# Kernel tuning notes

Measured on AMD Instinct MI355X. Metric: run time of the kernel, lower is better.

## Reference

```python
import jax, jax.numpy as jnp
import numpy as np

# Sizes: N news nodes, E 'similar' edges, 768-d input, hidden 64, 4 heads, 2 HGT layers, 2 classes
N, E, F_IN, HID, H, L, C = 100000, 1600000, 768, 64, 4, 2, 2
D = HID // H  # per-head dim = 16


def setup_inputs() -> dict:
    key = jax.random.key(0)
    ks = jax.random.split(key, 16)
    s = 0.05
    nrm = lambda k, shape: jax.random.normal(k, shape, jnp.float32) * s
    return {
        "x": jax.random.normal(ks[0], (N, F_IN), jnp.float32),
        "edge_index": jax.random.randint(ks[1], (2, E), 0, N, jnp.int32),
        # input projection
        "Wp": nrm(ks[2], (F_IN, HID)), "bp": jnp.zeros((HID,), jnp.float32),
        # per-layer HGT params (stacked over L layers)
        "Wk": nrm(ks[3], (L, HID, HID)), "bk": jnp.zeros((L, HID), jnp.float32),
        "Wq": nrm(ks[4], (L, HID, HID)), "bq": jnp.zeros((L, HID), jnp.float32),
        "Wv": nrm(ks[5], (L, HID, HID)), "bv": jnp.zeros((L, HID), jnp.float32),
        "a_rel": nrm(ks[6], (L, H, D, D)),  # per-edge-type attention transform
        "m_rel": nrm(ks[7], (L, H, D, D)),  # per-edge-type message transform
        "p_rel": jnp.ones((L, H), jnp.float32),  # relation prior
        "Wo": nrm(ks[8], (L, HID, HID)), "bo": jnp.zeros((L, HID), jnp.float32),
        "skip": jnp.ones((L,), jnp.float32),
        # classifier MLP: 64 -> 32 -> 2
        "Wc1": nrm(ks[9], (HID, HID // 2)), "bc1": jnp.zeros((HID // 2,), jnp.float32),
        "Wc2": nrm(ks[10], (HID // 2, C)), "bc2": jnp.zeros((C,), jnp.float32),
    }


def _hgt_layer(h, src, dst, Wk, bk, Wq, bq, Wv, bv, a_rel, m_rel, p_rel, Wo, bo, skip):
    n = h.shape[0]
    k = (h @ Wk + bk).reshape(n, H, D)
    q = (h @ Wq + bq).reshape(n, H, D)
    v = (h @ Wv + bv).reshape(n, H, D)
    # per-edge attention logits: (k_src @ a_rel) . q_dst * p_rel / sqrt(D)
    k_e = jnp.einsum('ehd,hdf->ehf', k[src], a_rel)          # [E,H,D]
    alpha = jnp.einsum('ehf,ehf->eh', k_e, q[dst]) * p_rel / np.float32(np.sqrt(D))
    # segment softmax over incoming edges of each dst node
    mx = jax.ops.segment_max(alpha, dst, num_segments=n)     # [N,H]
    a = jnp.exp(alpha - mx[dst])
    denom = jax.ops.segment_sum(a, dst, num_segments=n)
    a = a / (denom[dst] + 1e-16)
    # messages + scatter-add aggregation
    msg = jnp.einsum('ehd,hdf->ehf', v[src], m_rel)          # [E,H,D]
    agg = jax.ops.segment_sum(a[..., None] * msg, dst, num_segments=n).reshape(n, HID)
    out = jax.nn.gelu(agg) @ Wo + bo
    g = jax.nn.sigmoid(skip)
    return g * out + (1.0 - g) * h  # skip connection (same dims)


def reference(x, edge_index, Wp, bp, Wk, bk, Wq, bq, Wv, bv, a_rel, m_rel, p_rel,
              Wo, bo, skip, Wc1, bc1, Wc2, bc2):
    src, dst = edge_index[0], edge_index[1]
    h = x @ Wp + bp
    for l in range(L):
        h = _hgt_layer(h, src, dst, Wk[l], bk[l], Wq[l], bq[l], Wv[l], bv[l],
                       a_rel[l], m_rel[l], p_rel[l], Wo[l], bo[l], skip[l])
        h = jax.nn.relu(h)  # dropout is identity in eval mode
    hc = jax.nn.relu(h @ Wc1 + bc1)
    return hc @ Wc2 + bc2  # [N, C] logits
```

## Files before the change

kernel.cpp:

```cpp
#include <hip/hip_runtime.h>
#include <hip/hip_fp16.h>
#include <math.h>


typedef __attribute__((ext_vector_type(8))) short bf16x8;
typedef __attribute__((ext_vector_type(4))) float f32x4;

__device__ __forceinline__ float gelu_t(float x) {
  const float c = 0.7978845608028654f;
  float t = tanhf(c * (x + 0.044715f * x * x * x));
  return 0.5f * x * (1.0f + t);
}

__device__ __forceinline__ void split1(float a, ushort& h, ushort& l) {
  unsigned u = __float_as_uint(a);
  unsigned uh = u & 0xffff0000u;
  float fl = a - __uint_as_float(uh);
  h = (ushort)(uh >> 16);
  l = (ushort)(__float_as_uint(fl) >> 16);
}

template<int CTRL>
__device__ __forceinline__ float row_ror_add(float v) {
  int r = __builtin_amdgcn_update_dpp(0, __float_as_int(v), CTRL, 0xF, 0xF, true);
  return v + __int_as_float(r);
}
__device__ __forceinline__ float red16(float v) {
  v = row_ror_add<0x121>(v);
  v = row_ror_add<0x122>(v);
  v = row_ror_add<0x124>(v);
  v = row_ror_add<0x128>(v);
  return v;
}

template<int K>
__global__ __launch_bounds__(256, 4)
void mfma_gemm(const float* __restrict__ A, int ldA,
               const ushort* __restrict__ Wt,
               const float* __restrict__ bias,
               float* __restrict__ outp, int ldOut, int nRows)
{
  constexpr int NCH = K / 32;
  __shared__ ushort sA[2 * 64 * 32];
  __shared__ ushort sB[2 * 64 * 32];
  const int tid = threadIdx.x;
  const int lane = tid & 63;
  const int wv = tid >> 6;
  const int m = lane & 15;
  const int q = lane >> 4;
  const int row0 = blockIdx.x * 64;
  const int colBlk = blockIdx.y * 64;

  const int srow = tid >> 2;
  const int skoff = (tid & 3) * 8;
  int gr = row0 + srow; if (gr >= nRows) gr = nRows - 1;
  const float* aBase = A + (size_t)gr * ldA + skoff;
  const float4* wBase = (const float4*)(Wt + (size_t)blockIdx.y * NCH * 4096);

  f32x4 acc[4];
#pragma unroll
  for (int ct = 0; ct < 4; ++ct) acc[ct] = (f32x4){0.f, 0.f, 0.f, 0.f};

  float4 a0 = *(const float4*)(aBase + 0);
  float4 a1 = *(const float4*)(aBase + 4);
  float4 b0 = wBase[tid * 2];
  float4 b1 = wBase[tid * 2 + 1];

#pragma clang loop unroll(disable)
  for (int ch = 0; ch < NCH; ++ch) {
    float4 na0 = a0, na1 = a1, nb0 = b0, nb1 = b1;
    if (ch + 1 < NCH) {
      na0 = *(const float4*)(aBase + (ch + 1) * 32);
      na1 = *(const float4*)(aBase + (ch + 1) * 32 + 4);
      const float4* wc = wBase + (size_t)(ch + 1) * 512;
      nb0 = wc[tid * 2];
      nb1 = wc[tid * 2 + 1];
    }
    float av[8] = {a0.x, a0.y, a0.z, a0.w, a1.x, a1.y, a1.z, a1.w};
    bf16x8 vh, vl;
#pragma unroll
    for (int j = 0; j < 8; ++j) {
      ushort h, l; split1(av[j], h, l);
      vh[j] = (short)h; vl[j] = (short)l;
    }
    __syncthreads();
    *(bf16x8*)(sA + srow * 32 + skoff) = vh;
    *(bf16x8*)(sA + 2048 + srow * 32 + skoff) = vl;
    ((float4*)sB)[tid * 2] = b0;
    ((float4*)sB)[tid * 2 + 1] = b1;
    __syncthreads();
    bf16x8 ah = *(const bf16x8*)(sA + (wv * 16 + m) * 32 + q * 8);
    bf16x8 al = *(const bf16x8*)(sA + 2048 + (wv * 16 + m) * 32 + q * 8);
#pragma unroll
    for (int ct = 0; ct < 4; ++ct) {
      bf16x8 bh = *(const bf16x8*)(sB + (ct * 16 + m) * 32 + q * 8);
      bf16x8 bl = *(const bf16x8*)(sB + 2048 + (ct * 16 + m) * 32 + q * 8);
      acc[ct] = __builtin_amdgcn_mfma_f32_16x16x32_bf16(ah, bh, acc[ct], 0, 0, 0);
      acc[ct] = __builtin_amdgcn_mfma_f32_16x16x32_bf16(ah, bl, acc[ct], 0, 0, 0);
      acc[ct] = __builtin_amdgcn_mfma_f32_16x16x32_bf16(al, bh, acc[ct], 0, 0, 0);
    }
    a0 = na0; a1 = na1; b0 = nb0; b1 = nb1;
  }

#pragma unroll
  for (int ct = 0; ct < 4; ++ct) {
    int c = colBlk + ct * 16 + m;
    float b = bias[c];
#pragma unroll
    for (int i = 0; i < 4; ++i) {
      int r = row0 + wv * 16 + q * 4 + i;
      if (r < nRows) outp[(size_t)r * ldOut + c] = acc[ct][i] + b;
    }
  }
}

template<int CB, int EPI>
__global__ __launch_bounds__(256, (CB == 1) ? 4 : 2)
void mfma_gemm_k64(const float* __restrict__ A,
                   const ushort* __restrict__ Wt,
                   const float* __restrict__ bias,
                   const float* __restrict__ Hprev,
                   const float* __restrict__ skipPtr,
                   float* __restrict__ outp, int ldOut, int nRows)
{
  __shared__ ushort sA[2 * 4096];
  __shared__ ushort sB[CB][2 * 4096];
  const int tid = threadIdx.x;
  const int lane = tid & 63;
  const int wv = tid >> 6;
  const int m = lane & 15;
  const int q = lane >> 4;
  const int row0 = blockIdx.x * 64;
  const int srow = tid >> 2;
  const int skoff = (tid & 3) * 8;
  int gr = row0 + srow; if (gr >= nRows) gr = nRows - 1;
  const float* aBase = A + (size_t)gr * 64 + skoff;
  const float4* wBase = (const float4*)Wt;

  float4 a0 = *(const float4*)(aBase + 0);
  float4 a1 = *(const float4*)(aBase + 4);
  float4 a2 = *(const float4*)(aBase + 32);
  float4 a3 = *(const float4*)(aBase + 36);
  float4 bb0[CB], bb1[CB], bb2[CB], bb3[CB];
#pragma unroll
  for (int cb = 0; cb < CB; ++cb) {
    bb0[cb] = wBase[(size_t)(cb * 2 + 0) * 512 + tid * 2];
    bb1[cb] = wBase[(size_t)(cb * 2 + 0) * 512 + tid * 2 + 1];
    bb2[cb] = wBase[(size_t)(cb * 2 + 1) * 512 + tid * 2];
    bb3[cb] = wBase[(size_t)(cb * 2 + 1) * 512 + tid * 2 + 1];
  }

  {
    float av[16] = {a0.x, a0.y, a0.z, a0.w, a1.x, a1.y, a1.z, a1.w,
                    a2.x, a2.y, a2.z, a2.w, a3.x, a3.y, a3.z, a3.w};
    if (EPI == 1) {
#pragma unroll
      for (int j = 0; j < 16; ++j) av[j] = gelu_t(av[j]);
    }
    bf16x8 vh0, vl0, vh1, vl1;
#pragma unroll
    for (int j = 0; j < 8; ++j) {
      ushort h, l; split1(av[j], h, l);
      vh0[j] = (short)h; vl0[j] = (short)l;
    }
#pragma unroll
    for (int j = 0; j < 8; ++j) {
      ushort h, l; split1(av[8 + j], h, l);
      vh1[j] = (short)h; vl1[j] = (short)l;
    }
    *(bf16x8*)(sA + srow * 32 + skoff) = vh0;
    *(bf16x8*)(sA + 2048 + srow * 32 + skoff) = vl0;
    *(bf16x8*)(sA + 4096 + srow * 32 + skoff) = vh1;
    *(bf16x8*)(sA + 4096 + 2048 + srow * 32 + skoff) = vl1;
  }
#pragma unroll
  for (int cb = 0; cb < CB; ++cb) {
    ((float4*)(sB[cb]))[tid * 2] = bb0[cb];
    ((float4*)(sB[cb]))[tid * 2 + 1] = bb1[cb];
    ((float4*)(sB[cb] + 4096))[tid * 2] = bb2[cb];
    ((float4*)(sB[cb] + 4096))[tid * 2 + 1] = bb3[cb];
  }
  __syncthreads();

  f32x4 acc[CB][4];
#pragma unroll
  for (int cb = 0; cb < CB; ++cb)
#pragma unroll
    for (int ct = 0; ct < 4; ++ct) acc[cb][ct] = (f32x4){0.f, 0.f, 0.f, 0.f};

  bf16x8 ah0 = *(const bf16x8*)(sA + (wv * 16 + m) * 32 + q * 8);
  bf16x8 al0 = *(const bf16x8*)(sA + 2048 + (wv * 16 + m) * 32 + q * 8);
  bf16x8 ah1 = *(const bf16x8*)(sA + 4096 + (wv * 16 + m) * 32 + q * 8);
  bf16x8 al1 = *(const bf16x8*)(sA + 4096 + 2048 + (wv * 16 + m) * 32 + q * 8);
#pragma unroll
  for (int cb = 0; cb < CB; ++cb) {
#pragma unroll
    for (int ct = 0; ct < 4; ++ct) {
      bf16x8 bh0 = *(const bf16x8*)(sB[cb] + (ct * 16 + m) * 32 + q * 8);
      bf16x8 bl0 = *(const bf16x8*)(sB[cb] + 2048 + (ct * 16 + m) * 32 + q * 8);
      acc[cb][ct] = __builtin_amdgcn_mfma_f32_16x16x32_bf16(ah0, bh0, acc[cb][ct], 0, 0, 0);
      acc[cb][ct] = __builtin_amdgcn_mfma_f32_16x16x32_bf16(ah0, bl0, acc[cb][ct], 0, 0, 0);
      acc[cb][ct] = __builtin_amdgcn_mfma_f32_16x16x32_bf16(al0, bh0, acc[cb][ct], 0, 0, 0);
      bf16x8 bh1 = *(const bf16x8*)(sB[cb] + 4096 + (ct * 16 + m) * 32 + q * 8);
      bf16x8 bl1 = *(const bf16x8*)(sB[cb] + 4096 + 2048 + (ct * 16 + m) * 32 + q * 8);
      acc[cb][ct] = __builtin_amdgcn_mfma_f32_16x16x32_bf16(ah1, bh1, acc[cb][ct], 0, 0, 0);
      acc[cb][ct] = __builtin_amdgcn_mfma_f32_16x16x32_bf16(ah1, bl1, acc[cb][ct], 0, 0, 0);
      acc[cb][ct] = __builtin_amdgcn_mfma_f32_16x16x32_bf16(al1, bh1, acc[cb][ct], 0, 0, 0);
    }
  }

  if (EPI == 2) {
#pragma unroll
    for (int ct = 0; ct < 4; ++ct) {
      int c = ct * 16 + m;
      float bq_ = bias[c], bk_ = bias[64 + c], bv_ = bias[128 + c];
#pragma unroll
      for (int i = 0; i < 4; ++i) {
        int r = row0 + wv * 16 + q * 4 + i;
        if (r < nRows) {
          outp[(size_t)r * 128 + c] = acc[0][ct][i] + bq_;
          __half2 kv = __floats2half2_rn(acc[1][ct][i] + bk_, acc[2][ct][i] + bv_);
          *((__half2*)outp + (size_t)r * 128 + 64 + c) = kv;
        }
      }
    }
  } else {
    float g = 0.f, gi = 0.f;
    if (EPI == 1) { g = 1.0f / (1.0f + __expf(-skipPtr[0])); gi = 1.0f - g; }
#pragma unroll
    for (int cb = 0; cb < CB; ++cb) {
#pragma unroll
      for (int ct = 0; ct < 4; ++ct) {
        int c = cb * 64 + ct * 16 + m;
        float b = bias[c];
#pragma unroll
        for (int i = 0; i < 4; ++i) {
          int r = row0 + wv * 16 + q * 4 + i;
          if (r < nRows) {
            float o = acc[cb][ct][i] + b;
            if (EPI == 1) {
              float hp = Hprev[(size_t)r * 64 + c];
              o = fmaxf(g * o + gi * hp, 0.f);
            }
            outp[(size_t)r * ldOut + c] = o;
          }
        }
      }
    }
  }
}

__global__ void prep_weights(const float* __restrict__ W, int K, int C,
                             ushort* __restrict__ Wt)
{
  int idx = blockIdx.x * 256 + threadIdx.x;
  if (idx < K * C) {
    int k = idx / C, c = idx % C;
    ushort h, l; split1(W[idx], h, l);
    int cb = c >> 6, cc = c & 63, ch = k >> 5, kk = k & 31;
    size_t base = (size_t)(cb * (K >> 5) + ch) * 4096;
    Wt[base + cc * 32 + kk] = h;
    Wt[base + 2048 + cc * 32 + kk] = l;
  }
}

__global__ void fold_weights(const float* __restrict__ Wq, const float* __restrict__ bq,
                             const float* __restrict__ Wk, const float* __restrict__ bk,
                             const float* __restrict__ Wv, const float* __restrict__ bv,
                             const float* __restrict__ a_rel, const float* __restrict__ m_rel,
                             float* __restrict__ Wqkv, float* __restrict__ bqkv)
{
  int l = blockIdx.x;
  const float* wq = Wq + l * 4096; const float* wk = Wk + l * 4096; const float* wv = Wv + l * 4096;
  const float* bql = bq + l * 64;  const float* bkl = bk + l * 64;  const float* bvl = bv + l * 64;
  const float* ar = a_rel + l * 1024; const float* mr = m_rel + l * 1024;
  float* W = Wqkv + l * 64 * 192;  float* B = bqkv + l * 192;
  for (int t = threadIdx.x; t < 64 * 192; t += blockDim.x) {
    int i = t / 192, c = t % 192;
    float val;
    if (c < 64) {
      val = wq[i * 64 + c];
    } else if (c < 128) {
      int cc = c - 64, hh = cc >> 4, f = cc & 15;
      float s = 0.f;
      for (int d = 0; d < 16; ++d) s += wk[i * 64 + hh * 16 + d] * ar[hh * 256 + d * 16 + f];
      val = s;
    } else {
      int cc = c - 128, hh = cc >> 4, f = cc & 15;
      float s = 0.f;
      for (int d = 0; d < 16; ++d) s += wv[i * 64 + hh * 16 + d] * mr[hh * 256 + d * 16 + f];
      val = s;
    }
    W[i * 192 + c] = val;
  }
  for (int c = threadIdx.x; c < 192; c += blockDim.x) {
    float val;
    if (c < 64) {
      val = bql[c];
    } else if (c < 128) {
      int cc = c - 64, hh = cc >> 4, f = cc & 15;
      float s = 0.f;
      for (int d = 0; d < 16; ++d) s += bkl[hh * 16 + d] * ar[hh * 256 + d * 16 + f];
      val = s;
    } else {
      int cc = c - 128, hh = cc >> 4, f = cc & 15;
      float s = 0.f;
      for (int d = 0; d < 16; ++d) s += bvl[hh * 16 + d] * mr[hh * 256 + d * 16 + f];
      val = s;
    }
    B[c] = val;
  }
}

__global__ void hist_kernel(const int* __restrict__ dst, int* __restrict__ counts, int E) {
  int e = blockIdx.x * 256 + threadIdx.x;
  if (e < E) atomicAdd(&counts[dst[e]], 1);
}

__global__ __launch_bounds__(256)
void scanA(int* __restrict__ counts, int* __restrict__ blockSums, int n) {
  __shared__ int sd[256];
  int tid = threadIdx.x;
  int base = blockIdx.x * 1024 + tid * 4;
  int v[4];
#pragma unroll
  for (int j = 0; j < 4; ++j) v[j] = (base + j < n) ? counts[base + j] : 0;
  int t = v[0] + v[1] + v[2] + v[3];
  sd[tid] = t; __syncthreads();
  for (int offm = 1; offm < 256; offm <<= 1) {
    int adj = (tid >= offm) ? sd[tid - offm] : 0;
    __syncthreads();
    sd[tid] += adj;
    __syncthreads();
  }
  int run = sd[tid] - t;
#pragma unroll
  for (int j = 0; j < 4; ++j) {
    if (base + j < n) counts[base + j] = run;
    run += v[j];
  }
  if (tid == 255) blockSums[blockIdx.x] = sd[255];
}

__global__ void scanB(int* __restrict__ blockSums, int G, int* __restrict__ row_ptr, int n) {
  __shared__ int sd[128];
  int tid = threadIdx.x;
  int t = (tid < G) ? blockSums[tid] : 0;
  sd[tid] = t; __syncthreads();
  for (int offm = 1; offm < 128; offm <<= 1) {
    int adj = (tid >= offm) ? sd[tid - offm] : 0;
    __syncthreads();
    sd[tid] += adj;
    __syncthreads();
  }
  if (tid < G) blockSums[tid] = sd[tid] - t;
  if (tid == 127) row_ptr[n] = sd[127];
}

__global__ void scanC(const int* __restrict__ counts, const int* __restrict__ blockSums,
                      int* __restrict__ row_ptr, int* __restrict__ cursor, int n) {
  int idx = blockIdx.x * 256 + threadIdx.x;
  if (idx < n) {
    int v = counts[idx] + blockSums[idx >> 10];
    row_ptr[idx] = v;
    cursor[idx] = v;
  }
}

__global__ void scatter_kernel(const int* __restrict__ src, const int* __restrict__ dst,
                               int* __restrict__ cursor, int* __restrict__ csr_src, int E) {
  int e = blockIdx.x * 256 + threadIdx.x;
  if (e < E) {
    int d = dst[e];
    int pos = atomicAdd(&cursor[d], 1);
    csr_src[pos] = src[e];
  }
}

__global__ __launch_bounds__(256)
void edge_agg(const float* __restrict__ qkv, const int* __restrict__ row_ptr,
              const int* __restrict__ csr_src, const float* __restrict__ p_rel,
              float* __restrict__ agg, int n)
{
  int wid = blockIdx.x * 4 + (threadIdx.x >> 6);
  if (wid >= n) return;
  int lane = threadIdx.x & 63;
  int head = lane >> 4;
  float pr = p_rel[head] * 0.25f;
  float qv = qkv[(size_t)wid * 128 + lane] * pr;
  int e0 = __builtin_amdgcn_readfirstlane(row_ptr[wid]);
  int e1 = __builtin_amdgcn_readfirstlane(row_ptr[wid + 1]);
  const __half2* ktb = (const __half2*)qkv + 64 + lane;
  float num = 0.f, den = 0.f;
  for (int e = e0; e < e1; e += 8) {
    int last = e1 - 1;
    int i1 = (e + 1 < e1) ? e + 1 : last;
    int i2 = (e + 2 < e1) ? e + 2 : last;
    int i3 = (e + 3 < e1) ? e + 3 : last;
    int i4 = (e + 4 < e1) ? e + 4 : last;
    int i5 = (e + 5 < e1) ? e + 5 : last;
    int i6 = (e + 6 < e1) ? e + 6 : last;
    int i7 = (e + 7 < e1) ? e + 7 : last;
    int s0 = csr_src[e];
    int s1 = csr_src[i1];
    int s2 = csr_src[i2];
    int s3 = csr_src[i3];
    int s4 = csr_src[i4];
    int s5 = csr_src[i5];
    int s6 = csr_src[i6];
    int s7 = csr_src[i7];
    float2 f0 = __half22float2(ktb[(size_t)s0 * 128]);
    float2 f1 = __half22float2(ktb[(size_t)s1 * 128]);
    float2 f2 = __half22float2(ktb[(size_t)s2 * 128]);
    float2 f3 = __half22float2(ktb[(size_t)s3 * 128]);
    float2 f4 = __half22float2(ktb[(size_t)s4 * 128]);
    float2 f5 = __half22float2(ktb[(size_t)s5 * 128]);
    float2 f6 = __half22float2(ktb[(size_t)s6 * 128]);
    float2 f7 = __half22float2(ktb[(size_t)s7 * 128]);
    float p0 = red16(f0.x * qv);
    float p1 = red16(f1.x * qv);
    float p2 = red16(f2.x * qv);
    float p3 = red16(f3.x * qv);
    float p4 = red16(f4.x * qv);
    float p5 = red16(f5.x * qv);
    float p6 = red16(f6.x * qv);
    float p7 = red16(f7.x * qv);
    float w0 = __expf(p0);
    float w1 = (e + 1 < e1) ? __expf(p1) : 0.f;
    float w2 = (e + 2 < e1) ? __expf(p2) : 0.f;
    float w3 = (e + 3 < e1) ? __expf(p3) : 0.f;
    float w4 = (e + 4 < e1) ? __expf(p4) : 0.f;
    float w5 = (e + 5 < e1) ? __expf(p5) : 0.f;
    float w6 = (e + 6 < e1) ? __expf(p6) : 0.f;
    float w7 = (e + 7 < e1) ? __expf(p7) : 0.f;
    den += ((w0 + w1) + (w2 + w3)) + ((w4 + w5) + (w6 + w7));
    num = fmaf(w0, f0.y, num);
    num = fmaf(w1, f1.y, num);
    num = fmaf(w2, f2.y, num);
    num = fmaf(w3, f3.y, num);
    num = fmaf(w4, f4.y, num);
    num = fmaf(w5, f5.y, num);
    num = fmaf(w6, f6.y, num);
    num = fmaf(w7, f7.y, num);
  }
  agg[(size_t)wid * 64 + lane] = num / (den + 1e-16f);
}

__global__ __launch_bounds__(256)
void classifier(const float* __restrict__ h, const float* __restrict__ Wc1,
                const float* __restrict__ bc1, const float* __restrict__ Wc2,
                const float* __restrict__ bc2, float* __restrict__ out, int n)
{
  int row = blockIdx.x * 256 + threadIdx.x;
  if (row >= n) return;
  float hid[32];
#pragma unroll
  for (int j = 0; j < 32; ++j) hid[j] = bc1[j];
  const float* hr = h + (size_t)row * 64;
#pragma unroll 4
  for (int k = 0; k < 64; k += 4) {
    float4 x = *(const float4*)&hr[k];
#pragma unroll
    for (int j = 0; j < 32; ++j) {
      hid[j] += x.x * Wc1[k * 32 + j] + x.y * Wc1[(k + 1) * 32 + j]
              + x.z * Wc1[(k + 2) * 32 + j] + x.w * Wc1[(k + 3) * 32 + j];
    }
  }
  float o0 = bc2[0], o1 = bc2[1];
#pragma unroll
  for (int j = 0; j < 32; ++j) {
    float v = fmaxf(hid[j], 0.f);
    o0 += v * Wc2[j * 2 + 0];
    o1 += v * Wc2[j * 2 + 1];
  }
  *(float2*)&out[(size_t)row * 2] = make_float2(o0, o1);
}

extern "C" void kernel_launch(void* const* d_in, const int* in_sizes, int n_in,
                              void* d_out, int out_size, void* d_ws, size_t ws_size,
                              hipStream_t stream)
{
  const float* x     = (const float*)d_in[0];
  const int*  eidx   = (const int*)d_in[1];
  const float* Wp    = (const float*)d_in[2];
  const float* bp    = (const float*)d_in[3];
  const float* Wk    = (const float*)d_in[4];
  const float* bk    = (const float*)d_in[5];
  const float* Wq    = (const float*)d_in[6];
  const float* bq    = (const float*)d_in[7];
  const float* Wv    = (const float*)d_in[8];
  const float* bv    = (const float*)d_in[9];
  const float* a_rel = (const float*)d_in[10];
  const float* m_rel = (const float*)d_in[11];
  const float* p_rel = (const float*)d_in[12];
  const float* Wo    = (const float*)d_in[13];
  const float* bo    = (const float*)d_in[14];
  const float* skip  = (const float*)d_in[15];
  const float* Wc1   = (const float*)d_in[16];
  const float* bc1   = (const float*)d_in[17];
  const float* Wc2   = (const float*)d_in[18];
  const float* bc2   = (const float*)d_in[19];
  float* out = (float*)d_out;

  const int N = in_sizes[0] / 768;
  const int E = in_sizes[1] / 2;
  const int* srcIdx = eidx;
  const int* dstIdx = eidx + E;

  char* ws = (char*)d_ws;
  size_t off = 0;
  auto alloc = [&](size_t bytes) -> void* {
    void* p = ws + off;
    off = (off + bytes + 255) & ~(size_t)255;
    return p;
  };
  float* h     = (float*)alloc((size_t)N * 64 * 4);
  float* qkv   = (float*)alloc((size_t)N * 128 * 4);
  float* agg   = (float*)alloc((size_t)N * 64 * 4);
  float* Wqkv  = (float*)alloc(2 * 64 * 192 * 4);
  float* bqkv  = (float*)alloc(2 * 192 * 4);
  int* row_ptr = (int*)alloc((size_t)(N + 1) * 4);
  int* cursor  = (int*)alloc((size_t)N * 4);
  int* counts  = (int*)alloc((size_t)N * 4);
  int* blockSums = (int*)alloc(512 * 4);
  int* csr_src = (int*)alloc((size_t)E * 4);
  ushort* WtP   = (ushort*)alloc((size_t)64 * 768 * 2 * 2);
  ushort* WtQKV = (ushort*)alloc((size_t)2 * 192 * 64 * 2 * 2);
  ushort* WtO   = (ushort*)alloc((size_t)2 * 64 * 64 * 2 * 2);
  (void)ws_size; (void)n_in; (void)out_size;

  hipMemsetAsync(counts, 0, (size_t)N * 4, stream);

  fold_weights<<<2, 256, 0, stream>>>(Wq, bq, Wk, bk, Wv, bv, a_rel, m_rel, Wqkv, bqkv);

  prep_weights<<<(768 * 64 + 255) / 256, 256, 0, stream>>>(Wp, 768, 64, WtP);
  for (int l = 0; l < 2; ++l) {
    prep_weights<<<(64 * 192 + 255) / 256, 256, 0, stream>>>(
        Wqkv + l * 64 * 192, 64, 192, WtQKV + (size_t)l * 192 * 64 * 2);
    prep_weights<<<(64 * 64 + 255) / 256, 256, 0, stream>>>(
        Wo + l * 4096, 64, 64, WtO + (size_t)l * 64 * 64 * 2);
  }

  mfma_gemm<768><<<dim3((N + 63) / 64, 1), 256, 0, stream>>>(
      x, 768, WtP, bp, h, 64, N);

  hist_kernel<<<(E + 255) / 256, 256, 0, stream>>>(dstIdx, counts, E);
  int G = (N + 1023) / 1024;
  scanA<<<G, 256, 0, stream>>>(counts, blockSums, N);
  scanB<<<1, 128, 0, stream>>>(blockSums, G, row_ptr, N);
  scanC<<<(N + 255) / 256, 256, 0, stream>>>(counts, blockSums, row_ptr, cursor, N);
  scatter_kernel<<<(E + 255) / 256, 256, 0, stream>>>(srcIdx, dstIdx, cursor, csr_src, E);

  for (int l = 0; l < 2; ++l) {
    mfma_gemm_k64<3, 2><<<(N + 63) / 64, 256, 0, stream>>>(
        h, WtQKV + (size_t)l * 192 * 64 * 2, bqkv + l * 192,
        nullptr, nullptr, qkv, 128, N);
    edge_agg<<<(N + 3) / 4, 256, 0, stream>>>(qkv, row_ptr, csr_src, p_rel + l * 4, agg, N);
    mfma_gemm_k64<1, 1><<<(N + 63) / 64, 256, 0, stream>>>(
        agg, WtO + (size_t)l * 64 * 64 * 2, bo + l * 64, h, skip + l, h, 64, N);
  }

  classifier<<<(N + 255) / 256, 256, 0, stream>>>(h, Wc1, bc1, Wc2, bc2, out, N);
}
```

Baseline: 937.9 us.

## Fuse weight prep kernels, widen input GEMM K-step, split QKV GEMM

Merges the weight folding, per-matrix bf16 split/transpose kernels and the counts memset into one prep_all launch to cut launch overhead. The 768-K input projection now stages 64 K-elements per iteration, halving barriers, but loads weights without register prefetch. The fused QKV GEMM is split into a Q-only launch and a K/V launch with a higher occupancy hint. That adds one launch and rereads h, in exchange for lower register pressure.

```diff
diff --git a/kernel.cpp b/kernel.cpp
--- a/kernel.cpp
+++ b/kernel.cpp
@@ -40,22 +40,23 @@
                const float* __restrict__ bias,
                float* __restrict__ outp, int ldOut, int nRows)
 {
-  constexpr int NCH = K / 32;
-  __shared__ ushort sA[2 * 64 * 32];
-  __shared__ ushort sB[2 * 64 * 32];
+  constexpr int NSC = K / 64;
+  __shared__ ushort sA[8192];
+  __shared__ ushort sB[8192];
   const int tid = threadIdx.x;
   const int lane = tid & 63;
   const int wv = tid >> 6;
   const int m = lane & 15;
   const int q = lane >> 4;
   const int row0 = blockIdx.x * 64;
-  const int colBlk = blockIdx.y * 64;
 
   const int srow = tid >> 2;
-  const int skoff = (tid & 3) * 8;
+  const int sq = tid & 3;
+  const int sub = sq >> 1;
+  const int koff = (sq & 1) * 16;
   int gr = row0 + srow; if (gr >= nRows) gr = nRows - 1;
-  const float* aBase = A + (size_t)gr * ldA + skoff;
-  const float4* wBase = (const float4*)(Wt + (size_t)blockIdx.y * NCH * 4096);
+  const float* aBase = A + (size_t)gr * ldA + sq * 16;
+  const float4* wBase = (const float4*)Wt;
 
   f32x4 acc[4];
 #pragma unroll
@@ -63,48 +64,73 @@
 
   float4 a0 = *(const float4*)(aBase + 0);
   float4 a1 = *(const float4*)(aBase + 4);
-  float4 b0 = wBase[tid * 2];
-  float4 b1 = wBase[tid * 2 + 1];
+  float4 a2 = *(const float4*)(aBase + 8);
+  float4 a3 = *(const float4*)(aBase + 12);
 
 #pragma clang loop unroll(disable)
-  for (int ch = 0; ch < NCH; ++ch) {
-    float4 na0 = a0, na1 = a1, nb0 = b0, nb1 = b1;
-    if (ch + 1 < NCH) {
-      na0 = *(const float4*)(aBase + (ch + 1) * 32);
-      na1 = *(const float4*)(aBase + (ch + 1) * 32 + 4);
-      const float4* wc = wBase + (size_t)(ch + 1) * 512;
-      nb0 = wc[tid * 2];
-      nb1 = wc[tid * 2 + 1];
-    }
-    float av[8] = {a0.x, a0.y, a0.z, a0.w, a1.x, a1.y, a1.z, a1.w};
-    bf16x8 vh, vl;
+  for (int ch = 0; ch < NSC; ++ch) {
+    float4 b0 = wBase[ch * 1024 + tid * 4 + 0];
+    float4 b1 = wBase[ch * 1024 + tid * 4 + 1];
+    float4 b2 = wBase[ch * 1024 + tid * 4 + 2];
+    float4 b3 = wBase[ch * 1024 + tid * 4 + 3];
+    float4 na0 = a0, na1 = a1, na2 = a2, na3 = a3;
+    if (ch + 1 < NSC) {
+      na0 = *(const float4*)(aBase + (ch + 1) * 64 + 0);
+      na1 = *(const float4*)(aBase + (ch + 1) * 64 + 4);
+      na2 = *(const float4*)(aBase + (ch + 1) * 64 + 8);
+      na3 = *(const float4*)(aBase + (ch + 1) * 64 + 12);
+    }
+    float av[16] = {a0.x, a0.y, a0.z, a0.w, a1.x, a1.y, a1.z, a1.w,
+                    a2.x, a2.y, a2.z, a2.w, a3.x, a3.y, a3.z, a3.w};
+    bf16x8 vh0, vl0, vh1, vl1;
 #pragma unroll
     for (int j = 0; j < 8; ++j) {
       ushort h, l; split1(av[j], h, l);
-      vh[j] = (short)h; vl[j] = (short)l;
+      vh0[j] = (short)h; vl0[j] = (short)l;
+    }
+#pragma unroll
+    for (int j = 0; j < 8; ++j) {
+      ushort h, l; split1(av[8 + j], h, l);
+      vh1[j] = (short)h; vl1[j] = (short)l;
     }
     __syncthreads();
-    *(bf16x8*)(sA + srow * 32 + skoff) = vh;
-    *(bf16x8*)(sA + 2048 + srow * 32 + skoff) = vl;
-    ((float4*)sB)[tid * 2] = b0;
-    ((float4*)sB)[tid * 2 + 1] = b1;
+    {
+      ushort* sAp = sA + sub * 4096 + srow * 32 + koff;
+      *(bf16x8*)(sAp) = vh0;
+      *(bf16x8*)(sAp + 8) = vh1;
+      *(bf16x8*)(sAp + 2048) = vl0;
+      *(bf16x8*)(sAp + 2048 + 8) = vl1;
+    }
+    ((float4*)sB)[tid * 4 + 0] = b0;
+    ((float4*)sB)[tid * 4 + 1] = b1;
+    ((float4*)sB)[tid * 4 + 2] = b2;
+    ((float4*)sB)[tid * 4 + 3] = b3;
     __syncthreads();
-    bf16x8 ah = *(const bf16x8*)(sA + (wv * 16 + m) * 32 + q * 8);
-    bf16x8 al = *(const bf16x8*)(sA + 2048 + (wv * 16 + m) * 32 + q * 8);
+    const int fo = (wv * 16 + m) * 32 + q * 8;
+    bf16x8 ah0 = *(const bf16x8*)(sA + fo);
+    bf16x8 al0 = *(const bf16x8*)(sA + 2048 + fo);
+    bf16x8 ah1 = *(const bf16x8*)(sA + 4096 + fo);
+    bf16x8 al1 = *(const bf16x8*)(sA + 4096 + 2048 + fo);
 #pragma unroll
     for (int ct = 0; ct < 4; ++ct) {
-      bf16x8 bh = *(const bf16x8*)(sB + (ct * 16 + m) * 32 + q * 8);
-      bf16x8 bl = *(const bf16x8*)(sB + 2048 + (ct * 16 + m) * 32 + q * 8);
-      acc[ct] = __builtin_amdgcn_mfma_f32_16x16x32_bf16(ah, bh, acc[ct], 0, 0, 0);
-      acc[ct] = __builtin_amdgcn_mfma_f32_16x16x32_bf16(ah, bl, acc[ct], 0, 0, 0);
-      acc[ct] = __builtin_amdgcn_mfma_f32_16x16x32_bf16(al, bh, acc[ct], 0, 0, 0);
-    }
-    a0 = na0; a1 = na1; b0 = nb0; b1 = nb1;
+      const int bo = (ct * 16 + m) * 32 + q * 8;
+      bf16x8 bh0 = *(const bf16x8*)(sB + bo);
+      bf16x8 bl0 = *(const bf16x8*)(sB + 2048 + bo);
+      acc[ct] = __builtin_amdgcn_mfma_f32_16x16x32_bf16(ah0, bh0, acc[ct], 0, 0, 0);
+      acc[ct] = __builtin_amdgcn_mfma_f32_16x16x32_bf16(ah0, bl0, acc[ct], 0, 0, 0);
+      acc[ct] = __builtin_amdgcn_mfma_f32_16x16x32_bf16(al0, bh0, acc[ct], 0, 0, 0);
+      bf16x8 bh1 = *(const bf16x8*)(sB + 4096 + bo);
+      bf16x8 bl1 = *(const bf16x8*)(sB + 4096 + 2048 + bo);
+      acc[ct] = __builtin_amdgcn_mfma_f32_16x16x32_bf16(ah1, bh1, acc[ct], 0, 0, 0);
+      acc[ct] = __builtin_amdgcn_mfma_f32_16x16x32_bf16(ah1, bl1, acc[ct], 0, 0, 0);
+      acc[ct] = __builtin_amdgcn_mfma_f32_16x16x32_bf16(al1, bh1, acc[ct], 0, 0, 0);
+    }
+    a0 = na0; a1 = na1; a2 = na2; a3 = na3;
   }
 
 #pragma unroll
   for (int ct = 0; ct < 4; ++ct) {
-    int c = colBlk + ct * 16 + m;
+    int c = ct * 16 + m;
     float b = bias[c];
 #pragma unroll
     for (int i = 0; i < 4; ++i) {
@@ -115,7 +141,7 @@
 }
 
 template<int CB, int EPI>
-__global__ __launch_bounds__(256, (CB == 1) ? 4 : 2)
+__global__ __launch_bounds__(256, (CB == 1) ? 4 : 3)
 void mfma_gemm_k64(const float* __restrict__ A,
                    const ushort* __restrict__ Wt,
                    const float* __restrict__ bias,
@@ -213,13 +239,12 @@
 #pragma unroll
     for (int ct = 0; ct < 4; ++ct) {
       int c = ct * 16 + m;
-      float bq_ = bias[c], bk_ = bias[64 + c], bv_ = bias[128 + c];
+      float bk_ = bias[c], bv_ = bias[64 + c];
 #pragma unroll
       for (int i = 0; i < 4; ++i) {
         int r = row0 + wv * 16 + q * 4 + i;
         if (r < nRows) {
-          outp[(size_t)r * 128 + c] = acc[0][ct][i] + bq_;
-          __half2 kv = __floats2half2_rn(acc[1][ct][i] + bk_, acc[2][ct][i] + bv_);
+          __half2 kv = __floats2half2_rn(acc[0][ct][i] + bk_, acc[1][ct][i] + bv_);
           *((__half2*)outp + (size_t)r * 128 + 64 + c) = kv;
         }
       }
@@ -250,65 +275,82 @@
   }
 }
 
-__global__ void prep_weights(const float* __restrict__ W, int K, int C,
-                             ushort* __restrict__ Wt)
+__global__ void prep_all(const float* __restrict__ Wp,
+                         const float* __restrict__ Wq, const float* __restrict__ bq,
+                         const float* __restrict__ Wk, const float* __restrict__ bk,
+                         const float* __restrict__ Wv, const float* __restrict__ bv,
+                         const float* __restrict__ a_rel, const float* __restrict__ m_rel,
+                         const float* __restrict__ Wo,
+                         ushort* __restrict__ WtP, ushort* __restrict__ WtQKV,
+                         ushort* __restrict__ WtO, float* __restrict__ bqkv,
+                         int* __restrict__ counts, int n)
 {
-  int idx = blockIdx.x * 256 + threadIdx.x;
-  if (idx < K * C) {
-    int k = idx / C, c = idx % C;
-    ushort h, l; split1(W[idx], h, l);
-    int cb = c >> 6, cc = c & 63, ch = k >> 5, kk = k & 31;
-    size_t base = (size_t)(cb * (K >> 5) + ch) * 4096;
-    Wt[base + cc * 32 + kk] = h;
-    Wt[base + 2048 + cc * 32 + kk] = l;
-  }
-}
-
-__global__ void fold_weights(const float* __restrict__ Wq, const float* __restrict__ bq,
-                             const float* __restrict__ Wk, const float* __restrict__ bk,
-                             const float* __restrict__ Wv, const float* __restrict__ bv,
-                             const float* __restrict__ a_rel, const float* __restrict__ m_rel,
-                             float* __restrict__ Wqkv, float* __restrict__ bqkv)
-{
-  int l = blockIdx.x;
-  const float* wq = Wq + l * 4096; const float* wk = Wk + l * 4096; const float* wv = Wv + l * 4096;
-  const float* bql = bq + l * 64;  const float* bkl = bk + l * 64;  const float* bvl = bv + l * 64;
-  const float* ar = a_rel + l * 1024; const float* mr = m_rel + l * 1024;
-  float* W = Wqkv + l * 64 * 192;  float* B = bqkv + l * 192;
-  for (int t = threadIdx.x; t < 64 * 192; t += blockDim.x) {
-    int i = t / 192, c = t % 192;
+  int i = blockIdx.x * 256 + threadIdx.x;
+  if (i < 49152) {
+    int k = i >> 6, c = i & 63;
+    ushort h, l; split1(Wp[i], h, l);
+    size_t base = (size_t)(k >> 5) * 4096;
+    WtP[base + c * 32 + (k & 31)] = h;
+    WtP[base + 2048 + c * 32 + (k & 31)] = l;
+  } else if (i < 49152 + 24576) {
+    int j = i - 49152;
+    int l_ = j / 12288; j -= l_ * 12288;
+    int k = j / 192, c = j - k * 192;
     float val;
     if (c < 64) {
-      val = wq[i * 64 + c];
+      val = Wq[l_ * 4096 + k * 64 + c];
     } else if (c < 128) {
       int cc = c - 64, hh = cc >> 4, f = cc & 15;
+      const float* wk_ = Wk + l_ * 4096 + k * 64 + hh * 16;
+      const float* ar = a_rel + l_ * 1024 + hh * 256 + f;
       float s = 0.f;
-      for (int d = 0; d < 16; ++d) s += wk[i * 64 + hh * 16 + d] * ar[hh * 256 + d * 16 + f];
+      for (int d = 0; d < 16; ++d) s += wk_[d] * ar[d * 16];
       val = s;
     } else {
       int cc = c - 128, hh = cc >> 4, f = cc & 15;
+      const float* wv_ = Wv + l_ * 4096 + k * 64 + hh * 16;
+      const float* mr = m_rel + l_ * 1024 + hh * 256 + f;
       float s = 0.f;
-      for (int d = 0; d < 16; ++d) s += wv[i * 64 + hh * 16 + d] * mr[hh * 256 + d * 16 + f];
+      for (int d = 0; d < 16; ++d) s += wv_[d] * mr[d * 16];
       val = s;
     }
-    W[i * 192 + c] = val;
-  }
-  for (int c = threadIdx.x; c < 192; c += blockDim.x) {
+    ushort h, l; split1(val, h, l);
+    int cb = c >> 6, cc2 = c & 63;
+    size_t base = ((size_t)l_ * 6 + cb * 2 + (k >> 5)) * 4096;
+    WtQKV[base + cc2 * 32 + (k & 31)] = h;
+    WtQKV[base + 2048 + cc2 * 32 + (k & 31)] = l;
+  } else if (i < 49152 + 24576 + 8192) {
+    int j = i - 49152 - 24576;
+    int l_ = j >> 12; j &= 4095;
+    int k = j >> 6, c = j & 63;
+    ushort h, l; split1(Wo[l_ * 4096 + j], h, l);
+    size_t base = ((size_t)l_ * 2 + (k >> 5)) * 4096;
+    WtO[base + c * 32 + (k & 31)] = h;
+    WtO[base + 2048 + c * 32 + (k & 31)] = l;
+  } else if (i < 49152 + 24576 + 8192 + 384) {
+    int j = i - 49152 - 24576 - 8192;
+    int l_ = j / 192, c = j - l_ * 192;
     float val;
     if (c < 64) {
-      val = bql[c];
+      val = bq[l_ * 64 + c];
     } else if (c < 128) {
       int cc = c - 64, hh = cc >> 4, f = cc & 15;
+      const float* bk_ = bk + l_ * 64 + hh * 16;
+      const float* ar = a_rel + l_ * 1024 + hh * 256 + f;
       float s = 0.f;
-      for (int d = 0; d < 16; ++d) s += bkl[hh * 16 + d] * ar[hh * 256 + d * 16 + f];
+      for (int d = 0; d < 16; ++d) s += bk_[d] * ar[d * 16];
       val = s;
     } else {
       int cc = c - 128, hh = cc >> 4, f = cc & 15;
+      const float* bv_ = bv + l_ * 64 + hh * 16;
+      const float* mr = m_rel + l_ * 1024 + hh * 256 + f;
       float s = 0.f;
-      for (int d = 0; d < 16; ++d) s += bvl[hh * 16 + d] * mr[hh * 256 + d * 16 + f];
+      for (int d = 0; d < 16; ++d) s += bv_[d] * mr[d * 16];
       val = s;
     }
-    B[c] = val;
+    bqkv[l_ * 192 + c] = val;
+  } else if (i < 49152 + 24576 + 8192 + 384 + n) {
+    counts[i - (49152 + 24576 + 8192 + 384)] = 0;
   }
 }
 
@@ -517,7 +559,6 @@
   float* h     = (float*)alloc((size_t)N * 64 * 4);
   float* qkv   = (float*)alloc((size_t)N * 128 * 4);
   float* agg   = (float*)alloc((size_t)N * 64 * 4);
-  float* Wqkv  = (float*)alloc(2 * 64 * 192 * 4);
   float* bqkv  = (float*)alloc(2 * 192 * 4);
   int* row_ptr = (int*)alloc((size_t)(N + 1) * 4);
   int* cursor  = (int*)alloc((size_t)N * 4);
@@ -529,19 +570,12 @@
   ushort* WtO   = (ushort*)alloc((size_t)2 * 64 * 64 * 2 * 2);
   (void)ws_size; (void)n_in; (void)out_size;
 
-  hipMemsetAsync(counts, 0, (size_t)N * 4, stream);
-
-  fold_weights<<<2, 256, 0, stream>>>(Wq, bq, Wk, bk, Wv, bv, a_rel, m_rel, Wqkv, bqkv);
-
-  prep_weights<<<(768 * 64 + 255) / 256, 256, 0, stream>>>(Wp, 768, 64, WtP);
-  for (int l = 0; l < 2; ++l) {
-    prep_weights<<<(64 * 192 + 255) / 256, 256, 0, stream>>>(
-        Wqkv + l * 64 * 192, 64, 192, WtQKV + (size_t)l * 192 * 64 * 2);
-    prep_weights<<<(64 * 64 + 255) / 256, 256, 0, stream>>>(
-        Wo + l * 4096, 64, 64, WtO + (size_t)l * 64 * 64 * 2);
-  }
-
-  mfma_gemm<768><<<dim3((N + 63) / 64, 1), 256, 0, stream>>>(
+  int prepTotal = 49152 + 24576 + 8192 + 384 + N;
+  prep_all<<<(prepTotal + 255) / 256, 256, 0, stream>>>(
+      Wp, Wq, bq, Wk, bk, Wv, bv, a_rel, m_rel, Wo,
+      WtP, WtQKV, WtO, bqkv, counts, N);
+
+  mfma_gemm<768><<<(N + 63) / 64, 256, 0, stream>>>(
       x, 768, WtP, bp, h, 64, N);
 
   hist_kernel<<<(E + 255) / 256, 256, 0, stream>>>(dstIdx, counts, E);
@@ -552,12 +586,15 @@
   scatter_kernel<<<(E + 255) / 256, 256, 0, stream>>>(srcIdx, dstIdx, cursor, csr_src, E);
 
   for (int l = 0; l < 2; ++l) {
-    mfma_gemm_k64<3, 2><<<(N + 63) / 64, 256, 0, stream>>>(
-        h, WtQKV + (size_t)l * 192 * 64 * 2, bqkv + l * 192,
+    mfma_gemm_k64<1, 0><<<(N + 63) / 64, 256, 0, stream>>>(
+        h, WtQKV + (size_t)l * 24576, bqkv + l * 192,
+        nullptr, nullptr, qkv, 128, N);
+    mfma_gemm_k64<2, 2><<<(N + 63) / 64, 256, 0, stream>>>(
+        h, WtQKV + (size_t)l * 24576 + 8192, bqkv + l * 192 + 64,
         nullptr, nullptr, qkv, 128, N);
     edge_agg<<<(N + 3) / 4, 256, 0, stream>>>(qkv, row_ptr, csr_src, p_rel + l * 4, agg, N);
     mfma_gemm_k64<1, 1><<<(N + 63) / 64, 256, 0, stream>>>(
-        agg, WtO + (size_t)l * 64 * 64 * 2, bo + l * 64, h, skip + l, h, 64, N);
+        agg, WtO + (size_t)l * 8192, bo + l * 64, h, skip + l, h, 64, N);
   }
 
   classifier<<<(N + 255) / 256, 256, 0, stream>>>(h, Wc1, bc1, Wc2, bc2, out, N);
```

After: 906.5 us. 1.03x faster.
